# Kernel tuning notes

Measured on AMD Instinct MI355X. Metric: run time of the kernel, lower is better.

Reference implementation:

```python
import jax, jax.numpy as jnp
import numpy as np

V, E, H, K, VD, NH, FS, NL = 32000, 512, 512, 512, 512, 8, 2048, 6
B, MEM, SLEN = 256, 70, 11
MAXLEN = 71
THRESH = 1.0 - 0.1
EPS = 1e-6


def _timing_signal(length, channels):
    # Faithful to _gen_timing_signal (min_timescale=1, max_timescale=1e4)
    position = np.arange(length, dtype=np.float32)
    num_ts = channels // 2
    log_inc = np.log(1e4) / (num_ts - 1)
    inv_ts = np.exp(np.arange(num_ts, dtype=np.float32) * -log_inc)
    scaled = position[:, None] * inv_ts[None, :]
    sig = np.concatenate([np.sin(scaled), np.cos(scaled)], axis=1)
    return jnp.asarray(sig.reshape(1, length, channels), dtype=jnp.float32)

TIME_SIG = _timing_signal(MAXLEN, H)   # [1, 71, H]
POS_SIG = _timing_signal(NL, H)        # [1, NL, H]


def layer_norm(x, g, b):
    mu = x.mean(-1, keepdims=True)
    sd = x.std(-1, keepdims=True, ddof=1)  # torch std is unbiased
    return g * (x - mu) / (sd + EPS) + b


def conv1d(x, w, b):
    # x: [B,L,Cin]; w: torch layout [Cout,Cin,3]; 'both' padding -> same length
    y = jax.lax.conv_general_dilated(x, jnp.transpose(w, (2, 1, 0)), (1,), [(1, 1)],
                                     dimension_numbers=('NWC', 'WIO', 'NWC'))
    return y + b


def mha(x, wq, wk, wv, wo):
    Bx, L, _ = x.shape
    dk, dv = K // NH, VD // NH
    q = (x @ wq).reshape(Bx, L, NH, dk).transpose(0, 2, 1, 3) * dk ** -0.5
    k = (x @ wk).reshape(Bx, L, NH, dk).transpose(0, 2, 1, 3)
    v = (x @ wv).reshape(Bx, L, NH, dv).transpose(0, 2, 1, 3)
    a = jax.nn.softmax(jnp.einsum('bhqd,bhkd->bhqk', q, k), axis=-1)
    ctx = jnp.einsum('bhqk,bhkd->bhqd', a, v).transpose(0, 2, 1, 3).reshape(Bx, L, VD)
    return ctx @ wo


def enc_layer(x, p):
    xn = layer_norm(x, p['ln1_g'], p['ln1_b'])
    x = x + mha(xn, p['wq'], p['wk'], p['wv'], p['wo'])
    xn = layer_norm(x, p['ln2_g'], p['ln2_b'])
    y = conv1d(jax.nn.relu(conv1d(xn, p['c1_w'], p['c1_b'])), p['c2_w'], p['c2_b'])
    return x + y


def act_encode(x, p):
    Bx, L, _ = x.shape
    hp = jnp.zeros((Bx, L), x.dtype)
    rem = jnp.zeros((Bx, L), x.dtype)
    nu = jnp.zeros((Bx, L), x.dtype)
    prev = jnp.zeros_like(x)

    def step(carry, t):
        state, prev, hp, rem, nu = carry
        active = jnp.any((hp < THRESH) & (nu < NL))  # while-loop condition
        s = state + TIME_SIG[:, :L, :] + POS_SIG[:, t, :][:, None, :]
        pr = jax.nn.sigmoid(s @ p['p_w'] + p['p_b'])[..., 0]  # [B,L]
        still = (hp < 1.0).astype(x.dtype)
        tot = hp + pr * still
        new_halted = (tot > THRESH).astype(x.dtype) * still
        still2 = (tot <= THRESH).astype(x.dtype) * still
        hp2 = hp + pr * still2
        rem2 = rem + new_halted * (1.0 - hp2)
        hp2 = hp2 + new_halted * rem2
        nu2 = nu + still2 + new_halted
        uw = (pr * still2 + new_halted * rem2)[..., None]
        s2 = enc_layer(s, p)
        prev2 = s2 * uw + prev * (1.0 - uw)
        new = (s2, prev2, hp2, rem2, nu2)
        carry = jax.tree_util.tree_map(lambda a, b: jnp.where(active, b, a), carry, new)
        return carry, None

    (_, prev, hp, rem, nu), _ = jax.lax.scan(step, (x, prev, hp, rem, nu), jnp.arange(NL))
    return prev, rem, nu


def setup_inputs() -> dict:
    key = jax.random.key(0)
    ks = jax.random.split(key, 16)
    s = 0.02
    emb = jax.random.normal(ks[0], (V, E), jnp.float32) * s
    emb = emb.at[0].set(0.0)  # padding_idx=0
    return {
        'story': jax.random.randint(ks[1], (B, MEM, SLEN), 0, V),
        'query': jax.random.randint(ks[2], (B, SLEN), 0, V),
        'emb': emb,
        'mask_p': jnp.ones((11, E), jnp.float32),
        'proj_w': jax.random.normal(ks[3], (E, H), jnp.float32) * s,
        'ln1_g': jnp.ones((H,), jnp.float32), 'ln1_b': jnp.zeros((H,), jnp.float32),
        'wq': jax.random.normal(ks[4], (H, K), jnp.float32) * s,
        'wk': jax.random.normal(ks[5], (H, K), jnp.float32) * s,
        'wv': jax.random.normal(ks[6], (H, VD), jnp.float32) * s,
        'wo': jax.random.normal(ks[7], (VD, H), jnp.float32) * s,
        'c1_w': jax.random.normal(ks[8], (FS, H, 3), jnp.float32) * s,
        'c1_b': jnp.zeros((FS,), jnp.float32),
        'c2_w': jax.random.normal(ks[9], (H, FS, 3), jnp.float32) * s,
        'c2_b': jnp.zeros((H,), jnp.float32),
        'ln2_g': jnp.ones((H,), jnp.float32), 'ln2_b': jnp.zeros((H,), jnp.float32),
        'p_w': jax.random.normal(ks[10], (H, 1), jnp.float32) * s,
        'p_b': jnp.ones((1,), jnp.float32),  # bias init to 1 as in ACT_basic
        'out_b': jnp.zeros((V,), jnp.float32),
    }


def reference(story, query, emb, mask_p, proj_w, ln1_g, ln1_b, wq, wk, wv, wo,
              c1_w, c1_b, c2_w, c2_b, ln2_g, ln2_b, p_w, p_b, out_b):
    p = dict(ln1_g=ln1_g, ln1_b=ln1_b, wq=wq, wk=wk, wv=wv, wo=wo,
             c1_w=c1_w, c1_b=c1_b, c2_w=c2_w, c2_b=c2_b,
             ln2_g=ln2_g, ln2_b=ln2_b, p_w=p_w, p_b=p_b)
    S = story.shape[2]
    e = emb[story]                                         # [B,M,S,E]
    embed_story = jnp.sum(e * mask_p[:S][None, None], 2)   # [B,M,E]
    qe = emb[query]                                        # [B,S,E]
    embed_query = jnp.sum(qe[:, None] * mask_p[:query.shape[1]], 2)  # [B,1,E]
    x = jnp.concatenate([embed_story, embed_query], axis=1)          # [B,M+1,E]
    h = x @ proj_w  # proj_flag path (embedding_size == hidden_size)
    logit, rem, nu = act_encode(h, p)
    pooled = jnp.sum(logit, axis=1) / logit.shape[1]
    a_hat = pooled @ emb.T + out_b  # tied output weights
    return a_hat, jax.nn.softmax(a_hat, axis=1), rem, nu
```

## Files before the change

### kernel.cpp

```cpp
#include <hip/hip_runtime.h>
#include <hip/hip_bf16.h>
#include <math.h>


typedef unsigned short ushort_t;
using short8  = __attribute__((ext_vector_type(8))) short;
using floatx4 = __attribute__((ext_vector_type(4))) float;

#define B_   256
#define L_   71
#define H_   512
#define M_   (B_*L_)
#define MH_  9088
#define FS_  2048
#define V_   32000
#define NH_  8
#define DK_  64

__device__ inline ushort_t f2bf_rne(float f) {
    unsigned u = __float_as_uint(f);
    return (ushort_t)((u + 0x7FFFu + ((u >> 16) & 1u)) >> 16);
}

__device__ __forceinline__ void gload16(const void* g, void* l)
{
    __builtin_amdgcn_global_load_lds(
        (__attribute__((address_space(1))) unsigned int*)(g),
        (__attribute__((address_space(3))) unsigned int*)(l),
        16, 0, 0);
}

template<int MODE>
__global__ __launch_bounds__(256) void gemm_conv(
    const ushort_t* __restrict__ AH, const ushort_t* __restrict__ AL,
    int lda, int rowA, int rowG,
    const ushort_t* __restrict__ Bh, const ushort_t* __restrict__ Bl,
    int N, const float* __restrict__ bias,
    ushort_t* __restrict__ CoutH, ushort_t* __restrict__ CoutL,
    float* __restrict__ Cpart, long partStride, int cLen)
{
    __shared__ __attribute__((aligned(16))) short Ahs[4608], Als[4608];
    __shared__ __attribute__((aligned(16))) short Bhs[6144], Bls[6144];

    const int tid  = threadIdx.x;
    const int w    = tid >> 6, lane = tid & 63;

    int bn, by, z;
    if (MODE == 1) {
        const int id = blockIdx.x;
        const int l  = (id & 7) * 142 + (id >> 3);
        const int gp = l >> 2;
        by = gp % 71;
        const int zz = gp / 71;
        z  = zz >> 1;
        bn = (zz & 1) * 4 + (l & 3);
    } else {
        bn = blockIdx.x; by = blockIdx.y; z = 0;
    }
    const int cBeg = z * cLen;
    const int bm = by << 7;

    const int srow = lane & 15, skc = lane >> 4;
    const long aOff0 = (long)(rowA + bm - 1 + (w    ) * 16 + srow) * lda + skc * 8;
    const long aOff1 = (long)(rowA + bm - 1 + (w + 4) * 16 + srow) * lda + skc * 8;
    const long aOff2 = (long)(rowA + bm - 1 + 128 + srow) * lda + skc * 8;
    const long ldb = 3L * lda;
    const long bOff0 = (long)(bn * 64 + ((w    ) & 3) * 16 + srow) * ldb + ((w    ) >> 2) * lda + skc * 8;
    const long bOff1 = (long)(bn * 64 + ((w + 4) & 3) * 16 + srow) * ldb + ((w + 4) >> 2) * lda + skc * 8;
    const long bOff2 = (long)(bn * 64 + ((w + 8) & 3) * 16 + srow) * ldb + ((w + 8) >> 2) * lda + skc * 8;

    const int quad = lane >> 4, mr = lane & 15;
    const int boffL = quad * 128 + mr * 8;
    int aoffs[2][3];
    bool am0[2], am2[2];
    #pragma unroll
    for (int i = 0; i < 2; i++) {
        #pragma unroll
        for (int d = 0; d < 3; d++) {
            const int s = w * 32 + i * 16 + mr + d;
            aoffs[i][d] = (s >> 4) * 512 + quad * 128 + (s & 15) * 8;
        }
        const int lm = (bm + w * 32 + i * 16 + mr + rowG) % 71;
        am0[i] = (lm == 0);
        am2[i] = (lm == 70);
    }

    floatx4 acc[2][4] = {};

    const int cEnd = cBeg + cLen;
    for (int c0 = cBeg; c0 < cEnd; c0 += 32) {
        __syncthreads();
        gload16(AH + aOff0 + c0, Ahs + (w    ) * 512);
        gload16(AH + aOff1 + c0, Ahs + (w + 4) * 512);
        gload16(AL + aOff0 + c0, Als + (w    ) * 512);
        gload16(AL + aOff1 + c0, Als + (w + 4) * 512);
        if (w == 0) {
            gload16(AH + aOff2 + c0, Ahs + 8 * 512);
            gload16(AL + aOff2 + c0, Als + 8 * 512);
        }
        gload16(Bh + bOff0 + c0, Bhs + (w    ) * 512);
        gload16(Bh + bOff1 + c0, Bhs + (w + 4) * 512);
        gload16(Bh + bOff2 + c0, Bhs + (w + 8) * 512);
        gload16(Bl + bOff0 + c0, Bls + (w    ) * 512);
        gload16(Bl + bOff1 + c0, Bls + (w + 4) * 512);
        gload16(Bl + bOff2 + c0, Bls + (w + 8) * 512);
        __syncthreads();

        #pragma unroll
        for (int d = 0; d < 3; d++) {
            short8 bhf[4], blf[4];
            #pragma unroll
            for (int j = 0; j < 4; j++) {
                bhf[j] = *(const short8*)(Bhs + (d * 4 + j) * 512 + boffL);
                blf[j] = *(const short8*)(Bls + (d * 4 + j) * 512 + boffL);
            }
            #pragma unroll
            for (int i = 0; i < 2; i++) {
                short8 a_h = *(const short8*)(Ahs + aoffs[i][d]);
                short8 a_l = *(const short8*)(Als + aoffs[i][d]);
                if (d == 0) { if (am0[i]) { a_h = (short8)0; a_l = (short8)0; } }
                if (d == 2) { if (am2[i]) { a_h = (short8)0; a_l = (short8)0; } }
                #pragma unroll
                for (int j = 0; j < 4; j++) {
                    acc[i][j] = __builtin_amdgcn_mfma_f32_16x16x32_bf16(a_h, bhf[j], acc[i][j], 0, 0, 0);
                    acc[i][j] = __builtin_amdgcn_mfma_f32_16x16x32_bf16(a_l, bhf[j], acc[i][j], 0, 0, 0);
                    acc[i][j] = __builtin_amdgcn_mfma_f32_16x16x32_bf16(a_h, blf[j], acc[i][j], 0, 0, 0);
                }
            }
        }
    }

    #pragma unroll
    for (int j = 0; j < 4; j++) {
        const int gcol = bn * 64 + j * 16 + mr;
        const float bv = (MODE == 0) ? bias[gcol] : 0.f;
        #pragma unroll
        for (int i = 0; i < 2; i++) {
            #pragma unroll
            for (int r = 0; r < 4; r++) {
                const int grow = bm + w * 32 + i * 16 + quad * 4 + r;
                float v = acc[i][j][r];
                if (MODE == 0) {
                    v = fmaxf(v + bv, 0.f);
                    const long cidx = (long)grow * N + gcol;
                    ushort_t h = f2bf_rne(v);
                    float hf = __uint_as_float(((unsigned)h) << 16);
                    CoutH[cidx] = h;
                    CoutL[cidx] = f2bf_rne(v - hf);
                } else {
                    Cpart[(long)z * partStride + (long)grow * N + gcol] = v;
                }
            }
        }
    }
}

template<int TN>
__global__ __launch_bounds__(256) void gemm_s(
    const ushort_t* __restrict__ AH, const ushort_t* __restrict__ AL,
    int lda, int rowA,
    const ushort_t* __restrict__ Bh, const ushort_t* __restrict__ Bl,
    int N, int K,
    const float* __restrict__ bias, const float* residual,
    float alpha, int rowC, int outMode,
    float* Cout, ushort_t* CoutH, ushort_t* CoutL)
{
    constexpr int AF = (TN == 128) ? 4 : 2;
    __shared__ __attribute__((aligned(16))) short Ahs[4096], Als[4096];
    __shared__ __attribute__((aligned(16))) short Bhs[TN * 32], Bls[TN * 32];

    const int tid  = threadIdx.x;
    const int w    = tid >> 6, lane = tid & 63;
    const int bm = blockIdx.y << 7, bn = blockIdx.x * TN;

    const int srow = lane & 15;
    const int skc  = lane >> 4;
    const int ra0  = w * 16 + srow;
    const int ra1  = ra0 + 64;
    const ushort_t* pAh0 = AH + (long)(bm + ra0 + rowA) * lda + skc * 8;
    const ushort_t* pAl0 = AL + (long)(bm + ra0 + rowA) * lda + skc * 8;
    const ushort_t* pAh1 = AH + (long)(bm + ra1 + rowA) * lda + skc * 8;
    const ushort_t* pAl1 = AL + (long)(bm + ra1 + rowA) * lda + skc * 8;
    const ushort_t* pBh0 = Bh + (long)(bn + ra0) * K + skc * 8;
    const ushort_t* pBl0 = Bl + (long)(bn + ra0) * K + skc * 8;
    const ushort_t* pBh1 = (TN == 128) ? (Bh + (long)(bn + ra1) * K + skc * 8) : nullptr;
    const ushort_t* pBl1 = (TN == 128) ? (Bl + (long)(bn + ra1) * K + skc * 8) : nullptr;

    const int quad = lane >> 4, mr = lane & 15;
    const int wrM   = (TN == 128) ? ((w >> 1) << 6) : (w << 5);
    const int wcN   = (TN == 128) ? ((w & 1) << 6) : 0;
    const int agrp0 = (TN == 128) ? ((w >> 1) << 2) : (w << 1);
    const int bgrp0 = (TN == 128) ? ((w & 1) << 2) : 0;
    const int foff  = quad * 128 + mr * 8;

    floatx4 acc[AF][4] = {};

    for (int k0 = 0; k0 < K; k0 += 32) {
        __syncthreads();
        gload16(pAh0 + k0, Ahs + w * 512);
        gload16(pAh1 + k0, Ahs + (w + 4) * 512);
        gload16(pAl0 + k0, Als + w * 512);
        gload16(pAl1 + k0, Als + (w + 4) * 512);
        if constexpr (TN == 128) {
            gload16(pBh0 + k0, Bhs + w * 512);
            gload16(pBh1 + k0, Bhs + (w + 4) * 512);
            gload16(pBl0 + k0, Bls + w * 512);
            gload16(pBl1 + k0, Bls + (w + 4) * 512);
        } else {
            gload16(pBh0 + k0, Bhs + w * 512);
            gload16(pBl0 + k0, Bls + w * 512);
        }
        __syncthreads();

        short8 ah[AF], al[AF], bh[4], bl[4];
        #pragma unroll
        for (int i = 0; i < AF; i++) {
            ah[i] = *(const short8*)(Ahs + (agrp0 + i) * 512 + foff);
            al[i] = *(const short8*)(Als + (agrp0 + i) * 512 + foff);
        }
        #pragma unroll
        for (int j = 0; j < 4; j++) {
            bh[j] = *(const short8*)(Bhs + (bgrp0 + j) * 512 + foff);
            bl[j] = *(const short8*)(Bls + (bgrp0 + j) * 512 + foff);
        }
        #pragma unroll
        for (int i = 0; i < AF; i++)
        #pragma unroll
        for (int j = 0; j < 4; j++) {
            acc[i][j] = __builtin_amdgcn_mfma_f32_16x16x32_bf16(ah[i], bh[j], acc[i][j], 0, 0, 0);
            acc[i][j] = __builtin_amdgcn_mfma_f32_16x16x32_bf16(al[i], bh[j], acc[i][j], 0, 0, 0);
            acc[i][j] = __builtin_amdgcn_mfma_f32_16x16x32_bf16(ah[i], bl[j], acc[i][j], 0, 0, 0);
        }
    }

    #pragma unroll
    for (int j = 0; j < 4; j++) {
        const int gcol = bn + wcN + j * 16 + mr;
        const float bv = bias ? bias[gcol] : 0.f;
        #pragma unroll
        for (int i = 0; i < AF; i++) {
            #pragma unroll
            for (int r = 0; r < 4; r++) {
                const int grow = bm + wrM + i * 16 + quad * 4 + r;
                const long crow = (long)grow + rowC;
                float v = acc[i][j][r] * alpha + bv;
                if (residual) v += residual[crow * N + gcol];
                const long cidx = crow * (long)N + gcol;
                if (outMode == 2) {
                    ushort_t h = f2bf_rne(v);
                    float hf = __uint_as_float(((unsigned)h) << 16);
                    CoutH[cidx] = h;
                    CoutL[cidx] = f2bf_rne(v - hf);
                } else {
                    Cout[cidx] = v;
                }
            }
        }
    }
}

__global__ __launch_bounds__(256) void conv2_reduce(
    const float* __restrict__ part, long partStride,
    const float* __restrict__ bias, float* __restrict__ trunk,
    float* __restrict__ prev, const float* __restrict__ uw, int rowC)
{
    const long n4 = (long)MH_ * H_ / 4;
    long i4 = (long)blockIdx.x * 256 + threadIdx.x;
    if (i4 >= n4) return;
    const long row  = i4 >> 7;
    const float4 p0 = ((const float4*)part)[i4];
    const float4 p1 = ((const float4*)(part + partStride))[i4];
    const float4 b4 = ((const float4*)bias)[i4 & 127];
    const long  ti  = (long)rowC * 128 + i4;
    float4 tv = ((const float4*)trunk)[ti];
    float4 v;
    v.x = p0.x + p1.x + b4.x + tv.x;
    v.y = p0.y + p1.y + b4.y + tv.y;
    v.z = p0.z + p1.z + b4.z + tv.z;
    v.w = p0.w + p1.w + b4.w + tv.w;
    ((float4*)trunk)[ti] = v;
    const float u = uw[rowC + row];
    float4 pv = ((const float4*)prev)[ti];
    pv.x = v.x * u + pv.x * (1.f - u);
    pv.y = v.y * u + pv.y * (1.f - u);
    pv.z = v.z * u + pv.z * (1.f - u);
    pv.w = v.w * u + pv.w * (1.f - u);
    ((float4*)prev)[ti] = pv;
}

__global__ __launch_bounds__(256) void sig_prep(float* __restrict__ T, float* __restrict__ P)
{
    int i = blockIdx.x * 256 + threadIdx.x;
    const int NT = 71 * 512;
    if (i >= NT + 6 * 512) return;
    int pos, c, idx;
    float* dst;
    if (i < NT) { pos = i >> 9; c = i & 511; dst = T; idx = i; }
    else        { int j = i - NT; pos = j >> 9; c = j & 511; dst = P; idx = j; }
    const float loginc = 0.036119766f;
    int jj = c & 255;
    float inv = expf(-(float)jj * loginc);
    float arg = (float)pos * inv;
    dst[idx] = (c < 256) ? sinf(arg) : cosf(arg);
}

__global__ __launch_bounds__(256) void gate_kernel(
    const float* __restrict__ hp, const float* __restrict__ nu, int* __restrict__ flag)
{
    int i = blockIdx.x * 256 + threadIdx.x;
    bool act = (i < M_) && (hp[i] < 0.9f) && (nu[i] < 6.0f);
    unsigned long long b = __ballot(act);
    if ((threadIdx.x & 63) == 0 && b) atomicOr(flag, 1);
}

__global__ __launch_bounds__(256) void s_pr_kernel(
    float* trunk, const float* __restrict__ Ttab, const float* __restrict__ Ptab,
    const float* __restrict__ p_w, const float* __restrict__ p_b,
    float* __restrict__ hp, float* __restrict__ rem, float* __restrict__ nu,
    float* __restrict__ uw, const int* __restrict__ flag, int t)
{
    const int row  = blockIdx.x * 4 + (threadIdx.x >> 6);
    const int lane = threadIdx.x & 63;
    const int l    = row % 71;
    float dot = 0.f;
    #pragma unroll
    for (int j = 0; j < 8; j++) {
        int c  = lane + 64 * j;
        float sv = trunk[(long)row * H_ + c] + Ttab[l * H_ + c] + Ptab[t * H_ + c];
        trunk[(long)row * H_ + c] = sv;
        dot += sv * p_w[c];
    }
    #pragma unroll
    for (int o = 32; o; o >>= 1) dot += __shfl_xor(dot, o);
    if (lane == 0) {
        if (flag[0]) {
            float pr = 1.f / (1.f + expf(-(dot + p_b[0])));
            float hp0 = hp[row], rem0 = rem[row], nu0 = nu[row];
            float still = (hp0 < 1.0f) ? 1.f : 0.f;
            float tot   = hp0 + pr * still;
            float nh    = ((tot > 0.9f) ? 1.f : 0.f) * still;
            float st2   = ((tot <= 0.9f) ? 1.f : 0.f) * still;
            float hp2   = hp0 + pr * st2;
            float rem2  = rem0 + nh * (1.f - hp2);
            hp2 += nh * rem2;
            hp[row] = hp2; rem[row] = rem2; nu[row] = nu0 + st2 + nh;
            uw[row] = pr * st2 + nh * rem2;
        } else {
            uw[row] = 0.f;
        }
    }
}

__global__ __launch_bounds__(256) void ln_kernel(
    const float* __restrict__ X, const float* __restrict__ g,
    const float* __restrict__ bb, ushort_t* __restrict__ outH,
    ushort_t* __restrict__ outL)
{
    const int row  = blockIdx.x * 4 + (threadIdx.x >> 6);
    const int lane = threadIdx.x & 63;
    const float* xr = X + (long)row * H_;
    float v[8];
    float s = 0.f;
    #pragma unroll
    for (int j = 0; j < 8; j++) { v[j] = xr[lane + 64 * j]; s += v[j]; }
    #pragma unroll
    for (int o = 32; o; o >>= 1) s += __shfl_xor(s, o);
    float mean = s * (1.f / 512.f);
    float q = 0.f;
    #pragma unroll
    for (int j = 0; j < 8; j++) { float d = v[j] - mean; q += d * d; }
    #pragma unroll
    for (int o = 32; o; o >>= 1) q += __shfl_xor(q, o);
    float sd  = sqrtf(q * (1.f / 511.f));
    float inv = 1.f / (sd + 1e-6f);
    #pragma unroll
    for (int j = 0; j < 8; j++) {
        int c = lane + 64 * j;
        float val = g[c] * (v[j] - mean) * inv + bb[c];
        ushort_t h = f2bf_rne(val);
        float hf = __uint_as_float(((unsigned)h) << 16);
        long idx = (long)row * H_ + c;
        outH[idx] = h;
        outL[idx] = f2bf_rne(val - hf);
    }
}

__global__ __launch_bounds__(256) void attn_kernel(
    const float* __restrict__ qkv, ushort_t* __restrict__ ctxH,
    ushort_t* __restrict__ ctxL)
{
    __shared__ float qs[L_ * 65];
    __shared__ float ks[L_ * 65];
    __shared__ float Ss[L_ * L_];
    const int tid = threadIdx.x;
    const int b = blockIdx.x >> 3, h = blockIdx.x & 7;
    const long qbase = (long)b * L_ * 1536 + h * DK_;
    for (int idx = tid; idx < L_ * DK_; idx += 256) {
        int i = idx >> 6, d = idx & 63;
        qs[i * 65 + d] = qkv[qbase + (long)i * 1536 + d];
        ks[i * 65 + d] = qkv[qbase + 512 + (long)i * 1536 + d];
    }
    __syncthreads();
    for (int idx = tid; idx < L_ * L_; idx += 256) {
        int i = idx / 71, j = idx % 71;
        const float* qr = qs + i * 65;
        const float* kr = ks + j * 65;
        float s0 = 0.f, s1 = 0.f, s2 = 0.f, s3 = 0.f;
        #pragma unroll
        for (int d = 0; d < 64; d += 4) {
            s0 += qr[d]     * kr[d];
            s1 += qr[d + 1] * kr[d + 1];
            s2 += qr[d + 2] * kr[d + 2];
            s3 += qr[d + 3] * kr[d + 3];
        }
        Ss[i * 71 + j] = (s0 + s1) + (s2 + s3);
    }
    __syncthreads();
    if (tid < L_) {
        float mx = -1e30f;
        for (int j = 0; j < L_; j++) mx = fmaxf(mx, Ss[tid * 71 + j]);
        float sm = 0.f;
        for (int j = 0; j < L_; j++) { float e = expf(Ss[tid * 71 + j] - mx); Ss[tid * 71 + j] = e; sm += e; }
        float inv = 1.f / sm;
        for (int j = 0; j < L_; j++) Ss[tid * 71 + j] *= inv;
    }
    for (int idx = tid; idx < L_ * DK_; idx += 256) {
        int i = idx >> 6, d = idx & 63;
        ks[i * 65 + d] = qkv[qbase + 1024 + (long)i * 1536 + d];
    }
    __syncthreads();
    const long obase = (long)b * L_ * H_ + h * DK_;
    for (int idx = tid; idx < L_ * DK_; idx += 256) {
        int i = idx >> 6, d = idx & 63;
        const float* sr = Ss + i * 71;
        float s0 = 0.f, s1 = 0.f;
        int j = 0;
        for (; j + 1 < L_; j += 2) {
            s0 += sr[j]     * ks[j * 65 + d];
            s1 += sr[j + 1] * ks[(j + 1) * 65 + d];
        }
        float s = s0 + s1 + sr[70] * ks[70 * 65 + d];
        ushort_t hh = f2bf_rne(s);
        float hf = __uint_as_float(((unsigned)hh) << 16);
        long o = obase + (long)i * H_ + d;
        ctxH[o] = hh;
        ctxL[o] = f2bf_rne(s - hf);
    }
}

__global__ __launch_bounds__(256) void embed_kernel(
    const int* __restrict__ story, const int* __restrict__ query,
    const float* __restrict__ emb, const float* __restrict__ mask,
    ushort_t* __restrict__ xH, ushort_t* __restrict__ xL)
{
    __shared__ int idx[11];
    const int row = blockIdx.x;
    const int b = row / 71, m = row % 71;
    const int tid = threadIdx.x;
    if (tid < 11)
        idx[tid] = (m < 70) ? story[((long)b * 70 + m) * 11 + tid]
                            : query[(long)b * 11 + tid];
    __syncthreads();
    for (int c = tid; c < H_; c += 256) {
        float acc = 0.f;
        #pragma unroll
        for (int s = 0; s < 11; s++)
            acc += emb[(long)idx[s] * H_ + c] * mask[s * H_ + c];
        ushort_t h = f2bf_rne(acc);
        float hf = __uint_as_float(((unsigned)h) << 16);
        long o = (long)row * H_ + c;
        xH[o] = h;
        xL[o] = f2bf_rne(acc - hf);
    }
}

__global__ __launch_bounds__(256) void wsplitT_kernel(
    const float* __restrict__ in, ushort_t* __restrict__ hi, ushort_t* __restrict__ lo,
    int R, int C, int rowOff, float scale)
{
    long i = (long)blockIdx.x * 256 + threadIdx.x;
    if (i < (long)R * C) {
        int r = (int)(i / C), c = (int)(i % C);
        float f = in[i] * scale;
        ushort_t h = f2bf_rne(f);
        float hf = __uint_as_float(((unsigned)h) << 16);
        hi[(long)(c + rowOff) * R + r] = h;
        lo[(long)(c + rowOff) * R + r] = f2bf_rne(f - hf);
    }
}

__global__ __launch_bounds__(256) void convw_split_kernel(
    const float* __restrict__ w, ushort_t* __restrict__ hi, ushort_t* __restrict__ lo,
    int N, int C)
{
    long i = (long)blockIdx.x * 256 + threadIdx.x;
    if (i < (long)N * C * 3) {
        int n = (int)(i / (3 * C));
        int r = (int)(i % (3 * C));
        int d = r / C, c = r % C;
        float f = w[((long)n * C + c) * 3 + d];
        ushort_t h = f2bf_rne(f);
        float hf = __uint_as_float(((unsigned)h) << 16);
        hi[i] = h;
        lo[i] = f2bf_rne(f - hf);
    }
}

__global__ __launch_bounds__(256) void esplit_kernel(
    const float* __restrict__ in, ushort_t* __restrict__ hi, ushort_t* __restrict__ lo,
    long n)
{
    long i = (long)blockIdx.x * 256 + threadIdx.x;
    if (i < n) {
        float f = in[i];
        ushort_t h = f2bf_rne(f);
        float hf = __uint_as_float(((unsigned)h) << 16);
        hi[i] = h;
        lo[i] = f2bf_rne(f - hf);
    }
}

__global__ __launch_bounds__(256) void zero_f32(float* __restrict__ p, long n)
{
    long i = (long)blockIdx.x * 256 + threadIdx.x;
    if (i < n) p[i] = 0.f;
}

__global__ __launch_bounds__(256) void pooled_kernel(
    const float* __restrict__ prev, ushort_t* __restrict__ pH, ushort_t* __restrict__ pL)
{
    int i = blockIdx.x * 256 + threadIdx.x;
    int b = i >> 9, c = i & 511;
    float s = 0.f;
    for (int l = 0; l < L_; l++) s += prev[((long)b * L_ + l) * H_ + c];
    float p = s / 71.0f;
    ushort_t h = f2bf_rne(p);
    float hf = __uint_as_float(((unsigned)h) << 16);
    pH[i] = h;
    pL[i] = f2bf_rne(p - hf);
}

__global__ __launch_bounds__(256) void softmax_kernel(
    const float* __restrict__ ah, float* __restrict__ out)
{
    __shared__ float red[256];
    const int b = blockIdx.x, tid = threadIdx.x;
    const float* a = ah + (long)b * V_;
    float mx = -1e30f;
    for (int i = tid; i < V_; i += 256) mx = fmaxf(mx, a[i]);
    red[tid] = mx; __syncthreads();
    for (int o = 128; o; o >>= 1) { if (tid < o) red[tid] = fmaxf(red[tid], red[tid + o]); __syncthreads(); }
    mx = red[0]; __syncthreads();
    float s = 0.f;
    for (int i = tid; i < V_; i += 256) s += expf(a[i] - mx);
    red[tid] = s; __syncthreads();
    for (int o = 128; o; o >>= 1) { if (tid < o) red[tid] += red[tid + o]; __syncthreads(); }
    float inv = 1.f / red[0];
    float* o_ = out + (long)b * V_;
    for (int i = tid; i < V_; i += 256) o_[i] = expf(a[i] - mx) * inv;
}

__global__ __launch_bounds__(256) void tails_kernel(
    const float* __restrict__ rem, const float* __restrict__ nu, float* __restrict__ out)
{
    int i = blockIdx.x * 256 + threadIdx.x;
    if (i < M_) {
        out[i] = rem[i];
        out[M_ + i] = nu[i];
    }
}

extern "C" void kernel_launch(void* const* d_in, const int* in_sizes, int n_in,
                              void* d_out, int out_size, void* d_ws, size_t ws_size,
                              hipStream_t stream)
{
    const int*   story  = (const int*)d_in[0];
    const int*   query  = (const int*)d_in[1];
    const float* emb    = (const float*)d_in[2];
    const float* mask_p = (const float*)d_in[3];
    const float* proj_w = (const float*)d_in[4];
    const float* ln1_g  = (const float*)d_in[5];
    const float* ln1_b  = (const float*)d_in[6];
    const float* wq     = (const float*)d_in[7];
    const float* wk     = (const float*)d_in[8];
    const float* wv     = (const float*)d_in[9];
    const float* wo     = (const float*)d_in[10];
    const float* c1_w   = (const float*)d_in[11];
    const float* c1_b   = (const float*)d_in[12];
    const float* c2_w   = (const float*)d_in[13];
    const float* c2_b   = (const float*)d_in[14];
    const float* ln2_g  = (const float*)d_in[15];
    const float* ln2_b  = (const float*)d_in[16];
    const float* p_w    = (const float*)d_in[17];
    const float* p_b    = (const float*)d_in[18];
    const float* out_b  = (const float*)d_in[19];
    float* outp = (float*)d_out;

    char* wsb = (char*)d_ws;
    size_t off = 0;
    auto alloc = [&](size_t bytes) -> void* {
        void* p = wsb + off;
        off = (off + bytes + 255) & ~(size_t)255;
        return p;
    };
    const long ROWE = (long)M_ * H_;

    float* trunkF = (float*)alloc(ROWE * 4);
    float* prevF  = (float*)alloc(ROWE * 4);
    char*  poolC  = (char*)alloc(4L * ROWE * 4);
    float* hpF    = (float*)alloc((long)M_ * 4 * 4 + 64);
    float* remF   = hpF + M_;
    float* nuF    = hpF + 2 * M_;
    float* uwF    = hpF + 3 * M_;
    int*   flags  = (int*)(hpF + 4 * M_);
    ushort_t* projH = (ushort_t*)alloc((long)H_ * H_ * 2);
    ushort_t* projL = (ushort_t*)alloc((long)H_ * H_ * 2);
    ushort_t* wqkvH = (ushort_t*)alloc((long)3 * H_ * H_ * 2);
    ushort_t* wqkvL = (ushort_t*)alloc((long)3 * H_ * H_ * 2);
    ushort_t* woH   = (ushort_t*)alloc((long)H_ * H_ * 2);
    ushort_t* woL   = (ushort_t*)alloc((long)H_ * H_ * 2);
    ushort_t* W1H   = (ushort_t*)alloc((long)FS_ * 3 * H_ * 2);
    ushort_t* W1L   = (ushort_t*)alloc((long)FS_ * 3 * H_ * 2);
    ushort_t* W2H   = (ushort_t*)alloc((long)H_ * 3 * FS_ * 2);
    ushort_t* W2L   = (ushort_t*)alloc((long)H_ * 3 * FS_ * 2);
    ushort_t* pooledH = (ushort_t*)alloc((long)B_ * H_ * 2);
    ushort_t* pooledL = (ushort_t*)alloc((long)B_ * H_ * 2);
    float* Ttab     = (float*)alloc((long)L_ * H_ * 4);
    float* Ptab     = (float*)alloc(6L * H_ * 4);

    ushort_t* xnH = (ushort_t*)poolC;
    ushort_t* xnL = xnH + ROWE;
    float* qkvF = (float*)(poolC + ROWE * 4);
    ushort_t* ctxH = xnH;
    ushort_t* ctxL = xnL;
    ushort_t* xn2H = (ushort_t*)poolC;
    ushort_t* xn2L = xn2H + ROWE;
    ushort_t* y1H  = (ushort_t*)(poolC + ROWE * 4);
    ushort_t* y1L  = y1H + (long)MH_ * FS_;
    float* partF   = (float*)(poolC + ROWE * 4 + (long)MH_ * FS_ * 4);
    ushort_t* xembH = (ushort_t*)poolC;
    ushort_t* xembL = xembH + ROWE;
    ushort_t* embH = (ushort_t*)poolC;
    ushort_t* embL = embH + (long)V_ * H_;

    dim3 blk(256);

    zero_f32<<<dim3((unsigned)((ROWE + 255) / 256)), blk, 0, stream>>>(prevF, ROWE);
    zero_f32<<<dim3((3 * M_ + 255) / 256), blk, 0, stream>>>(hpF, 3 * M_);
    zero_f32<<<dim3(1), blk, 0, stream>>>((float*)flags, 16);
    sig_prep<<<dim3(154), blk, 0, stream>>>(Ttab, Ptab);

    wsplitT_kernel<<<dim3(1024), blk, 0, stream>>>(proj_w, projH, projL, H_, H_, 0, 1.f);
    wsplitT_kernel<<<dim3(1024), blk, 0, stream>>>(wq, wqkvH, wqkvL, H_, H_, 0, 0.125f);
    wsplitT_kernel<<<dim3(1024), blk, 0, stream>>>(wk, wqkvH, wqkvL, H_, H_, 512, 1.f);
    wsplitT_kernel<<<dim3(1024), blk, 0, stream>>>(wv, wqkvH, wqkvL, H_, H_, 1024, 1.f);
    wsplitT_kernel<<<dim3(1024), blk, 0, stream>>>(wo, woH, woL, H_, H_, 0, 1.f);
    convw_split_kernel<<<dim3(12288), blk, 0, stream>>>(c1_w, W1H, W1L, FS_, H_);
    convw_split_kernel<<<dim3(12288), blk, 0, stream>>>(c2_w, W2H, W2L, H_, FS_);

    embed_kernel<<<dim3(M_), blk, 0, stream>>>(story, query, emb, mask_p, xembH, xembL);
    gemm_s<64><<<dim3(H_ / 64, M_ / 128), blk, 0, stream>>>(
        xembH, xembL, H_, 0, projH, projL, H_, H_,
        nullptr, nullptr, 1.f, 0, 0, trunkF, nullptr, nullptr);

    for (int t = 0; t < 6; t++) {
        gate_kernel<<<dim3(M_ / 256), blk, 0, stream>>>(hpF, nuF, flags + t);
        s_pr_kernel<<<dim3(M_ / 4), blk, 0, stream>>>(trunkF, Ttab, Ptab, p_w, p_b,
                                                      hpF, remF, nuF, uwF, flags + t, t);
        ln_kernel<<<dim3(M_ / 4), blk, 0, stream>>>(trunkF, ln1_g, ln1_b, xnH, xnL);
        gemm_s<128><<<dim3(1536 / 128, M_ / 128), blk, 0, stream>>>(
            xnH, xnL, H_, 0, wqkvH, wqkvL, 1536, H_,
            nullptr, nullptr, 1.f, 0, 0, qkvF, nullptr, nullptr);
        attn_kernel<<<dim3(B_ * NH_), blk, 0, stream>>>(qkvF, ctxH, ctxL);
        gemm_s<64><<<dim3(H_ / 64, M_ / 128), blk, 0, stream>>>(
            ctxH, ctxL, H_, 0, woH, woL, H_, H_,
            nullptr, trunkF, 1.f, 0, 0, trunkF, nullptr, nullptr);
        ln_kernel<<<dim3(M_ / 4), blk, 0, stream>>>(trunkF, ln2_g, ln2_b, xn2H, xn2L);
        for (int half = 0; half < 2; half++) {
            int ro = half * MH_;
            gemm_conv<0><<<dim3(32, 71), blk, 0, stream>>>(
                xn2H, xn2L, H_, ro, ro, W1H, W1L, FS_,
                c1_b, y1H, y1L, nullptr, 0, 512);
            gemm_conv<1><<<dim3(1136), blk, 0, stream>>>(
                y1H, y1L, FS_, 0, ro, W2H, W2L, H_,
                nullptr, nullptr, nullptr, partF, (long)MH_ * H_, 1024);
            conv2_reduce<<<dim3((unsigned)((long)MH_ * H_ / 4 / 256)), blk, 0, stream>>>(
                partF, (long)MH_ * H_, c2_b, trunkF, prevF, uwF, ro);
        }
    }

    pooled_kernel<<<dim3(B_ * H_ / 256), blk, 0, stream>>>(prevF, pooledH, pooledL);
    esplit_kernel<<<dim3(64000), blk, 0, stream>>>(emb, embH, embL, (long)V_ * H_);
    gemm_s<64><<<dim3(V_ / 64, B_ / 128), blk, 0, stream>>>(
        pooledH, pooledL, H_, 0, embH, embL, V_, H_,
        out_b, nullptr, 1.f, 0, 0, outp, nullptr, nullptr);
    softmax_kernel<<<dim3(B_), blk, 0, stream>>>(outp, outp + (long)B_ * V_);
    tails_kernel<<<dim3((M_ + 255) / 256), blk, 0, stream>>>(remF, nuF, outp + 2L * B_ * V_);
}
```

Measured before the change: 8.220 ms.

## Vectorize and register-block attention kernel with parallel softmax

```diff
diff --git a/kernel.cpp b/kernel.cpp
--- a/kernel.cpp
+++ b/kernel.cpp
@@ -4,8 +4,9 @@
 
 
 typedef unsigned short ushort_t;
-using short8  = __attribute__((ext_vector_type(8))) short;
-using floatx4 = __attribute__((ext_vector_type(4))) float;
+using short8   = __attribute__((ext_vector_type(8))) short;
+using floatx4  = __attribute__((ext_vector_type(4))) float;
+using ushort4v = __attribute__((ext_vector_type(4))) unsigned short;
 
 #define B_   256
 #define L_   71
@@ -16,6 +17,9 @@
 #define V_   32000
 #define NH_  8
 #define DK_  64
+
+#define ATS  68
+#define SST  72
 
 __device__ inline ushort_t f2bf_rne(float f) {
     unsigned u = __float_as_uint(f);
@@ -389,62 +393,126 @@
     const float* __restrict__ qkv, ushort_t* __restrict__ ctxH,
     ushort_t* __restrict__ ctxL)
 {
-    __shared__ float qs[L_ * 65];
-    __shared__ float ks[L_ * 65];
-    __shared__ float Ss[L_ * L_];
+    __shared__ __attribute__((aligned(16))) float qs[L_ * ATS];
+    __shared__ __attribute__((aligned(16))) float ks[(L_ + 1) * ATS];
+    __shared__ __attribute__((aligned(16))) float Ss[L_ * SST];
+    __shared__ float rsum[L_ + 1];
     const int tid = threadIdx.x;
     const int b = blockIdx.x >> 3, h = blockIdx.x & 7;
     const long qbase = (long)b * L_ * 1536 + h * DK_;
-    for (int idx = tid; idx < L_ * DK_; idx += 256) {
-        int i = idx >> 6, d = idx & 63;
-        qs[i * 65 + d] = qkv[qbase + (long)i * 1536 + d];
-        ks[i * 65 + d] = qkv[qbase + 512 + (long)i * 1536 + d];
+
+    for (int idx = tid; idx < L_ * 16; idx += 256) {
+        const int i = idx >> 4, s4 = idx & 15;
+        const float4 qv = *(const float4*)(qkv + qbase + (long)i * 1536 + 4 * s4);
+        const float4 kv = *(const float4*)(qkv + qbase + 512 + (long)i * 1536 + 4 * s4);
+        *(float4*)(qs + i * ATS + 4 * s4) = qv;
+        *(float4*)(ks + i * ATS + 4 * s4) = kv;
+    }
+    if (tid < 16) {
+        float4 zz = {0.f, 0.f, 0.f, 0.f};
+        *(float4*)(ks + 71 * ATS + 4 * tid) = zz;
     }
     __syncthreads();
-    for (int idx = tid; idx < L_ * L_; idx += 256) {
-        int i = idx / 71, j = idx % 71;
-        const float* qr = qs + i * 65;
-        const float* kr = ks + j * 65;
+
+    for (int item = tid; item < 18 * L_; item += 256) {
+        const int jq = item / 71, i = item - jq * 71;
+        const float* qr = qs + i * ATS;
+        const float* k0 = ks + (4 * jq) * ATS;
         float s0 = 0.f, s1 = 0.f, s2 = 0.f, s3 = 0.f;
         #pragma unroll
-        for (int d = 0; d < 64; d += 4) {
-            s0 += qr[d]     * kr[d];
-            s1 += qr[d + 1] * kr[d + 1];
-            s2 += qr[d + 2] * kr[d + 2];
-            s3 += qr[d + 3] * kr[d + 3];
-        }
-        Ss[i * 71 + j] = (s0 + s1) + (s2 + s3);
+        for (int s4 = 0; s4 < 16; s4++) {
+            const float4 qv = *(const float4*)(qr + 4 * s4);
+            const float4 k0v = *(const float4*)(k0 + 4 * s4);
+            const float4 k1v = *(const float4*)(k0 + ATS + 4 * s4);
+            const float4 k2v = *(const float4*)(k0 + 2 * ATS + 4 * s4);
+            const float4 k3v = *(const float4*)(k0 + 3 * ATS + 4 * s4);
+            s0 += qv.x * k0v.x + qv.y * k0v.y + qv.z * k0v.z + qv.w * k0v.w;
+            s1 += qv.x * k1v.x + qv.y * k1v.y + qv.z * k1v.z + qv.w * k1v.w;
+            s2 += qv.x * k2v.x + qv.y * k2v.y + qv.z * k2v.z + qv.w * k2v.w;
+            s3 += qv.x * k3v.x + qv.y * k3v.y + qv.z * k3v.z + qv.w * k3v.w;
+        }
+        float4 sv; sv.x = s0; sv.y = s1; sv.z = s2; sv.w = s3;
+        *(float4*)(Ss + i * SST + 4 * jq) = sv;
     }
     __syncthreads();
-    if (tid < L_) {
-        float mx = -1e30f;
-        for (int j = 0; j < L_; j++) mx = fmaxf(mx, Ss[tid * 71 + j]);
-        float sm = 0.f;
-        for (int j = 0; j < L_; j++) { float e = expf(Ss[tid * 71 + j] - mx); Ss[tid * 71 + j] = e; sm += e; }
-        float inv = 1.f / sm;
-        for (int j = 0; j < L_; j++) Ss[tid * 71 + j] *= inv;
-    }
-    for (int idx = tid; idx < L_ * DK_; idx += 256) {
-        int i = idx >> 6, d = idx & 63;
-        ks[i * 65 + d] = qkv[qbase + 1024 + (long)i * 1536 + d];
+
+    for (int idx = tid; idx < L_ * 16; idx += 256) {
+        const int i = idx >> 4, s4 = idx & 15;
+        *(float4*)(ks + i * ATS + 4 * s4) =
+            *(const float4*)(qkv + qbase + 1024 + (long)i * 1536 + 4 * s4);
+    }
+
+    {
+        const int g = tid >> 2, r = tid & 3;
+        #pragma unroll
+        for (int half = 0; half < 2; half++) {
+            const int row = g + half * 64;
+            if (row < L_) {
+                float4 vals[5];
+                float mx = -1e30f;
+                #pragma unroll
+                for (int t = 0; t < 5; t++) {
+                    const int q = r + 4 * t;
+                    if (q < 18) {
+                        float4 v = *(const float4*)(Ss + row * SST + 4 * q);
+                        if (q == 17) v.w = -1e30f;
+                        vals[t] = v;
+                        mx = fmaxf(mx, fmaxf(fmaxf(v.x, v.y), fmaxf(v.z, v.w)));
+                    }
+                }
+                mx = fmaxf(mx, __shfl_xor(mx, 1));
+                mx = fmaxf(mx, __shfl_xor(mx, 2));
+                float sm = 0.f;
+                #pragma unroll
+                for (int t = 0; t < 5; t++) {
+                    const int q = r + 4 * t;
+                    if (q < 18) {
+                        float4 v = vals[t];
+                        v.x = expf(v.x - mx); v.y = expf(v.y - mx);
+                        v.z = expf(v.z - mx); v.w = expf(v.w - mx);
+                        sm += v.x + v.y + v.z + v.w;
+                        *(float4*)(Ss + row * SST + 4 * q) = v;
+                    }
+                }
+                sm += __shfl_xor(sm, 1);
+                sm += __shfl_xor(sm, 2);
+                if (r == 0) rsum[row] = 1.f / sm;
+            }
+        }
     }
     __syncthreads();
+
     const long obase = (long)b * L_ * H_ + h * DK_;
-    for (int idx = tid; idx < L_ * DK_; idx += 256) {
-        int i = idx >> 6, d = idx & 63;
-        const float* sr = Ss + i * 71;
-        float s0 = 0.f, s1 = 0.f;
-        int j = 0;
-        for (; j + 1 < L_; j += 2) {
-            s0 += sr[j]     * ks[j * 65 + d];
-            s1 += sr[j + 1] * ks[(j + 1) * 65 + d];
-        }
-        float s = s0 + s1 + sr[70] * ks[70 * 65 + d];
-        ushort_t hh = f2bf_rne(s);
-        float hf = __uint_as_float(((unsigned)hh) << 16);
-        long o = obase + (long)i * H_ + d;
-        ctxH[o] = hh;
-        ctxL[o] = f2bf_rne(s - hf);
+    for (int item = tid; item < L_ * 16; item += 256) {
+        const int i = item >> 4, dq = item & 15;
+        const float* sr = Ss + i * SST;
+        float ax = 0.f, ay = 0.f, az = 0.f, aw = 0.f;
+        #pragma unroll
+        for (int jq = 0; jq < 18; jq++) {
+            const float4 sv = *(const float4*)(sr + 4 * jq);
+            const float* v0 = ks + (4 * jq) * ATS + 4 * dq;
+            const float4 va = *(const float4*)(v0);
+            const float4 vb = *(const float4*)(v0 + ATS);
+            const float4 vc = *(const float4*)(v0 + 2 * ATS);
+            const float4 vd = *(const float4*)(v0 + 3 * ATS);
+            ax += sv.x * va.x + sv.y * vb.x + sv.z * vc.x + sv.w * vd.x;
+            ay += sv.x * va.y + sv.y * vb.y + sv.z * vc.y + sv.w * vd.y;
+            az += sv.x * va.z + sv.y * vb.z + sv.z * vc.z + sv.w * vd.z;
+            aw += sv.x * va.w + sv.y * vb.w + sv.z * vc.w + sv.w * vd.w;
+        }
+        const float rs = rsum[i];
+        float o[4] = {ax * rs, ay * rs, az * rs, aw * rs};
+        ushort4v hv, lv;
+        #pragma unroll
+        for (int c = 0; c < 4; c++) {
+            ushort_t hh = f2bf_rne(o[c]);
+            float hf = __uint_as_float(((unsigned)hh) << 16);
+            hv[c] = hh;
+            lv[c] = f2bf_rne(o[c] - hf);
+        }
+        const long oo = obase + (long)i * H_ + 4 * dq;
+        *(ushort4v*)(ctxH + oo) = hv;
+        *(ushort4v*)(ctxL + oo) = lv;
     }
 }
 
```

After: 7.821 ms. 4.9% less time.
